# Optimization experiments

Measured on AMD Instinct MI355X. Metric: run time of the kernel, lower is better.

## Reference

```python
import jax, jax.numpy as jnp
import numpy as np

EPS = 1e-5

def _bn(x, p):
    # p: (4, C) rows = gamma, beta, running_mean, running_var ; x: (B, C, H, W)
    g, b, m, v = p[0], p[1], p[2], p[3]
    sh = (1, -1, 1, 1)
    return (x - m.reshape(sh)) * (g.reshape(sh) * jax.lax.rsqrt(v.reshape(sh) + EPS)) + b.reshape(sh)

def _cba1(x, w, p):
    # 1x1 conv (no bias) + BN + ReLU
    return jax.nn.relu(_bn(jnp.einsum('oc,bchw->bohw', w, x), p))

def setup_inputs() -> dict:
    B, C, H, W = 2, 512, 128, 256
    CK, K, CO = 256, 19, 512
    key = jax.random.key(0)
    ks = jax.random.split(key, 10)
    def w(k, shape, fan):
        return jax.random.normal(k, shape, jnp.float32) * (fan ** -0.5)
    def bn(c):
        return jnp.stack([jnp.ones((c,), jnp.float32), jnp.zeros((c,), jnp.float32),
                          jnp.zeros((c,), jnp.float32), jnp.ones((c,), jnp.float32)])
    return {
        'x': jax.random.normal(ks[0], (B, C, H, W), jnp.float32),
        'proxy_feats': jax.random.normal(ks[1], (B, C, K, 1), jnp.float32),
        'wq1': w(ks[2], (CK, C), C),  'bnq1': bn(CK),
        'wq2': w(ks[3], (CK, CK), CK), 'bnq2': bn(CK),
        'wk1': w(ks[4], (CK, C), C),  'bnk1': bn(CK),
        'wk2': w(ks[5], (CK, CK), CK), 'bnk2': bn(CK),
        'wv':  w(ks[6], (CK, C), C),  'bnv':  bn(CK),
        'wout': w(ks[7], (C, CK), CK), 'bnout': bn(C),
        'wbot': w(ks[8], (CO, 2 * C, 3, 3), 2 * C * 9), 'bnbot': bn(CO),
    }

def reference(x, proxy_feats, wq1, wq2, wk1, wk2, wv, wout, wbot,
              bnq1, bnq2, bnk1, bnk2, bnv, bnout, bnbot):
    B, C, H, W = x.shape
    CK = wq1.shape[0]
    # --- ObjectContextBlock: pixel-region cross attention ---
    q = _cba1(_cba1(x, wq1, bnq1), wq2, bnq2)            # (B, CK, H, W)
    k = _cba1(_cba1(proxy_feats, wk1, bnk1), wk2, bnk2)  # (B, CK, K, 1)
    v = _cba1(proxy_feats, wv, bnv)                      # (B, CK, K, 1)
    q = q.reshape(B, CK, H * W)                          # (B, CK, N)
    k = k.reshape(B, CK, -1)                             # (B, CK, K)
    v = v.reshape(B, CK, -1)                             # (B, CK, K)
    sim = jnp.einsum('bcn,bck->bnk', q, k) * (CK ** -0.5)
    sim = jax.nn.softmax(sim, axis=-1)                   # (B, N, K)
    ctx = jnp.einsum('bnk,bck->bcn', sim, v).reshape(B, CK, H, W)
    ctx = _cba1(ctx, wout, bnout)                        # (B, C, H, W)
    # --- bottleneck: concat + 3x3 conv + BN + ReLU ---
    cat = jnp.concatenate([ctx, x], axis=1)              # (B, 2C, H, W)
    out = jax.lax.conv_general_dilated(cat, wbot, (1, 1), 'SAME',
                                       dimension_numbers=('NCHW', 'OIHW', 'NCHW'))
    return jax.nn.relu(_bn(out, bnbot))
```

## Files before the change

### kernel.cpp

```cpp
#include <hip/hip_runtime.h>
#include <cstdint>

#define EPS 1e-5f
#define PADW 258
#define PADROWS 33540
#define NPIX 32768

typedef __attribute__((ext_vector_type(8))) short bf16x8;
typedef __attribute__((ext_vector_type(4))) float f32x4;

__device__ __forceinline__ ushort f2bf(float f) {
  union { float f; uint32_t u; } v; v.f = f;
  uint32_t r = v.u + 0x7fffu + ((v.u >> 16) & 1u);
  return (ushort)(r >> 16);
}
__device__ __forceinline__ float bf2f(ushort h) {
  union { uint32_t u; float f; } v; v.u = ((uint32_t)h) << 16;
  return v.f;
}
__device__ __forceinline__ void gload_lds16(const void* g, void* lds) {
  __builtin_amdgcn_global_load_lds((__attribute__((address_space(1))) void*)g,
                                   (__attribute__((address_space(3))) void*)lds,
                                   16, 0, 0);
}

template <int BMODE, int OMODE>
__global__ __launch_bounds__(256) void mfma_gemm(
    const ushort* __restrict__ A, const ushort* __restrict__ B,
    const float* __restrict__ bn, void* __restrict__ OutV,
    int M, int K, int pitchB, int ciB, long strideB, int pitchO, long strideO) {
  const int lane = threadIdx.x & 63;
  const int wave = threadIdx.x >> 6;
  const int wm = (wave & 1) * 64;
  const int wn = (wave >> 1) * 64;
  const int m0 = blockIdx.y * 128;
  const int n0 = blockIdx.x * 128;
  const int z  = blockIdx.z;
  B += (size_t)z * strideB;

  const int h = n0 >> 8, w0 = n0 & 255;
  long prowB;
  if (BMODE == 0) prowB = n0;
  else            prowB = (long)(h + 1) * PADW + (w0 + 1);

  __shared__ __align__(16) ushort Asl[4 * 128 * 8];
  __shared__ __align__(16) ushort Bsl[4 * 128 * 8];

  f32x4 acc[4][4];
#pragma unroll
  for (int mt = 0; mt < 4; ++mt)
#pragma unroll
    for (int nt = 0; nt < 4; ++nt) acc[mt][nt] = (f32x4){0.f, 0.f, 0.f, 0.f};

  for (int k0 = 0; k0 < K; k0 += 32) {
#pragma unroll
    for (int i = 0; i < 2; ++i) {
      int s = wave * 2 + i;
      int c = s * 64 + lane;
      int mm = c & 127, ks = c >> 7;
      gload_lds16(A + (size_t)(m0 + mm) * K + (k0 + ks * 8), Asl + s * 512);
    }
    long rowb; int cib;
    if (BMODE == 2) {
      int tap = k0 >> 10;
      int dy = tap / 3 - 1, dx = tap % 3 - 1;
      rowb = prowB + dy * PADW + dx;
      cib  = k0 & 1023;
    } else {
      rowb = prowB;
      cib  = ciB + k0;
    }
#pragma unroll
    for (int i = 0; i < 2; ++i) {
      int s = wave * 2 + i;
      int c = s * 64 + lane;
      int nn = c & 127, ks = c >> 7;
      gload_lds16(B + (size_t)(rowb + nn) * pitchB + cib + ks * 8, Bsl + s * 512);
    }
    __syncthreads();
    bf16x8 af[4], bfr[4];
#pragma unroll
    for (int t = 0; t < 4; ++t) {
      af[t]  = *(const bf16x8*)(Asl + (((lane >> 4) * 128) + wm + t * 16 + (lane & 15)) * 8);
      bfr[t] = *(const bf16x8*)(Bsl + (((lane >> 4) * 128) + wn + t * 16 + (lane & 15)) * 8);
    }
#pragma unroll
    for (int mt = 0; mt < 4; ++mt)
#pragma unroll
      for (int nt = 0; nt < 4; ++nt)
        acc[mt][nt] = __builtin_amdgcn_mfma_f32_16x16x32_bf16(af[mt], bfr[nt], acc[mt][nt], 0, 0, 0);
    __syncthreads();
  }

  const int q4 = lane >> 4, col = lane & 15;
  float scv[16], bov[16];
#pragma unroll
  for (int mt = 0; mt < 4; ++mt)
#pragma unroll
    for (int r = 0; r < 4; ++r) {
      int m = m0 + wm + mt * 16 + q4 * 4 + r;
      float s = bn[m] * rsqrtf(bn[3 * M + m] + EPS);
      scv[mt * 4 + r] = s;
      bov[mt * 4 + r] = bn[M + m] - bn[2 * M + m] * s;
    }
  if (OMODE == 2) {
    float* Outf = (float*)OutV + (size_t)z * strideO;
#pragma unroll
    for (int mt = 0; mt < 4; ++mt)
#pragma unroll
      for (int r = 0; r < 4; ++r) {
        int m = m0 + wm + mt * 16 + q4 * 4 + r;
        float* rowp = Outf + (size_t)m * NPIX + n0 + wn;
#pragma unroll
        for (int nt = 0; nt < 4; ++nt)
          rowp[nt * 16 + col] = fmaxf(acc[mt][nt][r] * scv[mt * 4 + r] + bov[mt * 4 + r], 0.f);
      }
  } else {
    ushort* Outh = (ushort*)OutV + (size_t)z * strideO;
    long prowO = (OMODE == 0) ? (long)n0 : ((long)(h + 1) * PADW + (w0 + 1));
#pragma unroll
    for (int nt = 0; nt < 4; ++nt) {
      long row = prowO + wn + nt * 16 + col;
      ushort* p = Outh + (size_t)row * pitchO + m0 + wm;
#pragma unroll
      for (int mt = 0; mt < 4; ++mt) {
        ushort4 pk;
        pk.x = f2bf(fmaxf(acc[mt][nt][0] * scv[mt * 4 + 0] + bov[mt * 4 + 0], 0.f));
        pk.y = f2bf(fmaxf(acc[mt][nt][1] * scv[mt * 4 + 1] + bov[mt * 4 + 1], 0.f));
        pk.z = f2bf(fmaxf(acc[mt][nt][2] * scv[mt * 4 + 2] + bov[mt * 4 + 2], 0.f));
        pk.w = f2bf(fmaxf(acc[mt][nt][3] * scv[mt * 4 + 3] + bov[mt * 4 + 3], 0.f));
        *(ushort4*)(p + mt * 16 + q4 * 4) = pk;
      }
    }
  }
}

#define PXS  130
#define ROWC (PXS * 4)
#define BUFC (3 * ROWC)
__global__ __launch_bounds__(256, 3) void conv3x3_mfma(
    const ushort* __restrict__ W2, const ushort* __restrict__ cat,
    const float* __restrict__ bn, float* __restrict__ out) {
  const int tid  = threadIdx.x;
  const int lane = tid & 63;
  const int wave = tid >> 6;
  const int wm = (wave & 1) * 64;
  const int wn = (wave >> 1) * 64;
  const int m0 = (blockIdx.x & 3) * 128;
  const int n0 = (blockIdx.x >> 2) * 128;
  const int z  = blockIdx.z;
  const int h = n0 >> 8, w0 = n0 & 255;
  const long prow0 = (long)(h + 1) * PADW + (w0 + 1);
  const ushort* Bz = cat + (size_t)z * PADROWS * 1024;

  __shared__ __align__(16) ushort halo[2 * BUFC * 8];

  f32x4 acc[4][4];
#pragma unroll
  for (int mt = 0; mt < 4; ++mt)
#pragma unroll
    for (int nt = 0; nt < 4; ++nt) acc[mt][nt] = (f32x4){0.f, 0.f, 0.f, 0.f};

  long offs[7];
#pragma unroll
  for (int s = 0; s < 7; ++s) {
    int c = s * 256 + tid;
    if (c < BUFC) {
      int o = c & 3;
      int q = c >> 2;
      int p = q % PXS;
      int r = q / PXS;
      offs[s] = ((prow0 + (long)(r - 1) * PADW + (p - 1)) << 10) + o * 8;
    } else {
      offs[s] = -1;
    }
  }

  auto stage = [&](int buf, int ci0n) {
#pragma unroll
    for (int s = 0; s < 7; ++s)
      if (offs[s] >= 0)
        gload_lds16(Bz + offs[s] + ci0n,
                    halo + ((size_t)buf * BUFC + s * 256 + wave * 64) * 8);
  };

  const ushort* Alane = W2 + (size_t)(m0 + wm + (lane & 15)) * 32 + (lane >> 4) * 8;
  const int hlane = 4 * (wn + (lane & 15)) + (lane >> 4);

  stage(0, 0);
  __syncthreads();

  for (int it = 0; it < 32; ++it) {
    if (it < 31) stage((it + 1) & 1, (it + 1) * 32);

    const ushort* Ait = Alane + (size_t)it * (9 * 16384);
    const ushort* hb0 = halo + (size_t)(it & 1) * BUFC * 8;
#pragma unroll
    for (int t = 0; t < 9; ++t) {
      bf16x8 af[4];
#pragma unroll
      for (int mt = 0; mt < 4; ++mt)
        af[mt] = *(const bf16x8*)(Ait + (size_t)t * 16384 + mt * 512);
      const int hb = hlane + (t / 3) * ROWC + (t % 3) * 4;
#pragma unroll
      for (int nt = 0; nt < 4; ++nt) {
        bf16x8 bfr = *(const bf16x8*)(hb0 + (size_t)(hb + nt * 64) * 8);
#pragma unroll
        for (int mt = 0; mt < 4; ++mt)
          acc[mt][nt] = __builtin_amdgcn_mfma_f32_16x16x32_bf16(af[mt], bfr, acc[mt][nt], 0, 0, 0);
      }
    }
    __syncthreads();
  }

  const int q4 = lane >> 4, col = lane & 15;
  float* Outf = out + (size_t)z * 512 * NPIX;
#pragma unroll
  for (int mt = 0; mt < 4; ++mt)
#pragma unroll
    for (int r = 0; r < 4; ++r) {
      int m = m0 + wm + mt * 16 + q4 * 4 + r;
      float s  = bn[m] * rsqrtf(bn[3 * 512 + m] + EPS);
      float bo = bn[512 + m] - bn[2 * 512 + m] * s;
      float* rowp = Outf + (size_t)m * NPIX + n0 + wn;
#pragma unroll
      for (int nt = 0; nt < 4; ++nt)
        rowp[nt * 16 + col] = fmaxf(acc[mt][nt][r] * s + bo, 0.f);
    }
}

__global__ __launch_bounds__(64) void small_gemm_kernel(
    const float* __restrict__ Wm, const float* __restrict__ X,
    const float* __restrict__ bn, float* __restrict__ Y,
    int CO, int CI, int KC) {
  int co = blockIdx.x, b = blockIdx.y, kc = threadIdx.x;
  if (kc >= KC) return;
  const float* Xb = X + (size_t)b * CI * KC;
  float acc = 0.f;
  for (int c = 0; c < CI; ++c) acc += Wm[(size_t)co * CI + c] * Xb[(size_t)c * KC + kc];
  float s  = bn[co] * rsqrtf(bn[3 * CO + co] + EPS);
  float bs = bn[CO + co] - bn[2 * CO + co] * s;
  Y[((size_t)b * CO + co) * KC + kc] = fmaxf(acc * s + bs, 0.f);
}

__global__ __launch_bounds__(256) void attention_kernel(
    const ushort* __restrict__ qT, const float* __restrict__ Kp,
    const float* __restrict__ Vp, ushort* __restrict__ ctxT) {
  int b = blockIdx.y;
  int pix = blockIdx.x * 256 + threadIdx.x;
  __shared__ float ks[256][19], vs[256][19];
  for (int idx = threadIdx.x; idx < 256 * 19; idx += 256) {
    int c = idx / 19, kk = idx % 19;
    ks[c][kk] = Kp[((size_t)b * 256 + c) * 19 + kk];
    vs[c][kk] = Vp[((size_t)b * 256 + c) * 19 + kk];
  }
  __syncthreads();

  const ushort* qrow = qT + ((size_t)b * NPIX + pix) * 256;
  float sim[19];
#pragma unroll
  for (int kk = 0; kk < 19; ++kk) sim[kk] = 0.f;
  for (int c0 = 0; c0 < 256; c0 += 8) {
    uint4 raw = *(const uint4*)(qrow + c0);
    float qf[8] = {bf2f((ushort)(raw.x & 0xffff)), bf2f((ushort)(raw.x >> 16)),
                   bf2f((ushort)(raw.y & 0xffff)), bf2f((ushort)(raw.y >> 16)),
                   bf2f((ushort)(raw.z & 0xffff)), bf2f((ushort)(raw.z >> 16)),
                   bf2f((ushort)(raw.w & 0xffff)), bf2f((ushort)(raw.w >> 16))};
#pragma unroll
    for (int j = 0; j < 8; ++j)
#pragma unroll
      for (int kk = 0; kk < 19; ++kk) sim[kk] += qf[j] * ks[c0 + j][kk];
  }
  const float scale = 0.0625f;
  float mx = -1e30f;
#pragma unroll
  for (int kk = 0; kk < 19; ++kk) { sim[kk] *= scale; mx = fmaxf(mx, sim[kk]); }
  float denom = 0.f;
#pragma unroll
  for (int kk = 0; kk < 19; ++kk) { sim[kk] = __expf(sim[kk] - mx); denom += sim[kk]; }
  float inv = 1.f / denom;
#pragma unroll
  for (int kk = 0; kk < 19; ++kk) sim[kk] *= inv;

  ushort* crow = ctxT + ((size_t)b * NPIX + pix) * 256;
  for (int c0 = 0; c0 < 256; c0 += 8) {
    uint32_t o[4];
#pragma unroll
    for (int j = 0; j < 4; ++j) {
      float v0 = 0.f, v1 = 0.f;
#pragma unroll
      for (int kk = 0; kk < 19; ++kk) {
        v0 += sim[kk] * vs[c0 + j * 2][kk];
        v1 += sim[kk] * vs[c0 + j * 2 + 1][kk];
      }
      o[j] = (uint32_t)f2bf(v0) | ((uint32_t)f2bf(v1) << 16);
    }
    *(uint4*)(crow + c0) = make_uint4(o[0], o[1], o[2], o[3]);
  }
}

__global__ __launch_bounds__(256) void transpose_x_kernel(
    const float* __restrict__ x, ushort* __restrict__ cat) {
  int b = blockIdx.z, ci0 = blockIdx.y * 64, n0 = blockIdx.x * 64;
  __shared__ float t[64][65];
  const float* xb = x + ((size_t)b * 512 + ci0) * NPIX + n0;
  for (int i = 0; i < 16; ++i) {
    int idx = i * 256 + threadIdx.x;
    int c = idx >> 6, w = idx & 63;
    t[c][w] = xb[(size_t)c * NPIX + w];
  }
  __syncthreads();
  int h = n0 >> 8, w0 = n0 & 255;
  size_t pbase = ((size_t)b * PADROWS + (size_t)(h + 1) * PADW + (w0 + 1)) * 1024 + 512 + ci0;
  for (int i = 0; i < 16; ++i) {
    int idx = i * 256 + threadIdx.x;
    int n = idx >> 6, c = idx & 63;
    cat[pbase + (size_t)n * 1024 + c] = f2bf(t[c][n]);
  }
}

__global__ void convert_w_kernel(const float* __restrict__ in, ushort* __restrict__ out, int n) {
  int i = blockIdx.x * 256 + threadIdx.x;
  if (i < n) out[i] = f2bf(in[i]);
}
__global__ void repack_conv_w_kernel(const float* __restrict__ wbot, ushort* __restrict__ Wrb) {
  int idx = blockIdx.x * 256 + threadIdx.x;
  if (idx >= 512 * 9216) return;
  int ci_in = idx & 31;
  int r  = idx >> 5;
  int co = r & 511;
  int tt = r >> 9;
  int t = tt % 9, chunk = tt / 9;
  Wrb[idx] = f2bf(wbot[((size_t)co * 1024 + chunk * 32 + ci_in) * 9 + t]);
}

extern "C" void kernel_launch(void* const* d_in, const int* in_sizes, int n_in,
                              void* d_out, int out_size, void* d_ws, size_t ws_size,
                              hipStream_t stream) {
  const float* x     = (const float*)d_in[0];
  const float* proxy = (const float*)d_in[1];
  const float* wq1   = (const float*)d_in[2];
  const float* bnq1  = (const float*)d_in[3];
  const float* wq2   = (const float*)d_in[4];
  const float* bnq2  = (const float*)d_in[5];
  const float* wk1   = (const float*)d_in[6];
  const float* bnk1  = (const float*)d_in[7];
  const float* wk2   = (const float*)d_in[8];
  const float* bnk2  = (const float*)d_in[9];
  const float* wv    = (const float*)d_in[10];
  const float* bnv   = (const float*)d_in[11];
  const float* wout  = (const float*)d_in[12];
  const float* bnout = (const float*)d_in[13];
  const float* wbot  = (const float*)d_in[14];
  const float* bnbot = (const float*)d_in[15];
  float* out = (float*)d_out;

  const int B = 2, C = 512, CK = 256, KC = 19;
  char* ws = (char*)d_ws;
  const size_t catBytes = (size_t)B * PADROWS * 1024 * 2;
  ushort* cat  = (ushort*)ws;
  ushort* bufA = (ushort*)(ws + 137379840);
  ushort* bufB = (ushort*)(ws + 137379840 + 33554432);
  ushort* Wrb  = (ushort*)(ws + 204488704);
  ushort* wq1b = (ushort*)(ws + 213925888);
  ushort* wq2b = (ushort*)(ws + 214188032);
  ushort* woutb= (ushort*)(ws + 214319104);
  float*  k1   = (float*)(ws + 214581248);
  float*  k2   = k1 + (size_t)B * CK * KC;
  float*  vv   = k2 + (size_t)B * CK * KC;

  hipMemsetAsync(cat, 0, catBytes, stream);

  convert_w_kernel<<<(CK * C + 255) / 256, 256, 0, stream>>>(wq1, wq1b, CK * C);
  convert_w_kernel<<<(CK * CK + 255) / 256, 256, 0, stream>>>(wq2, wq2b, CK * CK);
  convert_w_kernel<<<(C * CK + 255) / 256, 256, 0, stream>>>(wout, woutb, C * CK);
  repack_conv_w_kernel<<<(512 * 9216 + 255) / 256, 256, 0, stream>>>(wbot, Wrb);

  small_gemm_kernel<<<dim3(CK, B), 64, 0, stream>>>(wk1, proxy, bnk1, k1, CK, C, KC);
  small_gemm_kernel<<<dim3(CK, B), 64, 0, stream>>>(wk2, k1, bnk2, k2, CK, CK, KC);
  small_gemm_kernel<<<dim3(CK, B), 64, 0, stream>>>(wv, proxy, bnv, vv, CK, C, KC);

  transpose_x_kernel<<<dim3(NPIX / 64, 8, B), 256, 0, stream>>>(x, cat);

  const long padStride = (long)PADROWS * 1024;
  const long nckStride = (long)NPIX * 256;

  mfma_gemm<1, 0><<<dim3(NPIX / 128, 2, B), 256, 0, stream>>>(
      wq1b, cat, bnq1, bufA, 256, 512, 1024, 512, padStride, 256, nckStride);
  mfma_gemm<0, 0><<<dim3(NPIX / 128, 2, B), 256, 0, stream>>>(
      wq2b, bufA, bnq2, bufB, 256, 256, 256, 0, nckStride, 256, nckStride);

  attention_kernel<<<dim3(NPIX / 256, B), 256, 0, stream>>>(bufB, k2, vv, bufA);

  mfma_gemm<0, 1><<<dim3(NPIX / 128, 4, B), 256, 0, stream>>>(
      woutb, bufA, bnout, cat, 512, 256, 256, 0, nckStride, 1024, padStride);

  conv3x3_mfma<<<dim3((NPIX / 128) * 4, 1, B), 256, 0, stream>>>(Wrb, cat, bnbot, out);
}
```

Baseline: 1.302 ms.

## Swizzle halo LDS layout and prefetch weight fragments in 3x3 conv loop

Adds an XOR swizzle on the 16-byte octet slot inside each halo pixel row, applied both when global data is staged into LDS and when B fragments are read back. This is meant to cut LDS bank conflicts. Weight A fragments are now loaded from global three taps ahead in a rotating buffer, and the async staging is wrapped in sched barriers so the loads overlap with MFMA work. MFMA bursts also run at raised wave priority. The cost is more registers, which may lower occupancy.

```diff
diff --git a/kernel.cpp b/kernel.cpp
--- a/kernel.cpp
+++ b/kernel.cpp
@@ -166,11 +166,12 @@
   for (int s = 0; s < 7; ++s) {
     int c = s * 256 + tid;
     if (c < BUFC) {
-      int o = c & 3;
+      int o_slot = c & 3;
       int q = c >> 2;
       int p = q % PXS;
       int r = q / PXS;
-      offs[s] = ((prow0 + (long)(r - 1) * PADW + (p - 1)) << 10) + o * 8;
+      int o_g = o_slot ^ ((p >> 1) & 3);
+      offs[s] = ((prow0 + (long)(r - 1) * PADW + (p - 1)) << 10) + o_g * 8;
     } else {
       offs[s] = -1;
     }
@@ -185,29 +186,55 @@
   };
 
   const ushort* Alane = W2 + (size_t)(m0 + wm + (lane & 15)) * 32 + (lane >> 4) * 8;
-  const int hlane = 4 * (wn + (lane & 15)) + (lane >> 4);
+
+  const int p0  = wn + (lane & 15);
+  const int oct = lane >> 4;
+  int hoff[12];
+#pragma unroll
+  for (int nt = 0; nt < 4; ++nt)
+#pragma unroll
+    for (int dx = 0; dx < 3; ++dx) {
+      int p = p0 + nt * 16 + dx;
+      hoff[nt * 3 + dx] = (p * 4 + (oct ^ ((p >> 1) & 3))) * 16;
+    }
 
   stage(0, 0);
   __syncthreads();
 
   for (int it = 0; it < 32; ++it) {
+    const ushort* Ait = Alane + (size_t)it * (9 * 16384);
+
+    bf16x8 af[3][4];
+#pragma unroll
+    for (int t = 0; t < 3; ++t)
+#pragma unroll
+      for (int mt = 0; mt < 4; ++mt)
+        af[t][mt] = *(const bf16x8*)(Ait + (size_t)t * 16384 + mt * 512);
+
+    __builtin_amdgcn_sched_barrier(0);
     if (it < 31) stage((it + 1) & 1, (it + 1) * 32);
-
-    const ushort* Ait = Alane + (size_t)it * (9 * 16384);
-    const ushort* hb0 = halo + (size_t)(it & 1) * BUFC * 8;
+    __builtin_amdgcn_sched_barrier(0);
+
+    const char* hb0 = (const char*)(halo + (size_t)(it & 1) * BUFC * 8);
 #pragma unroll
     for (int t = 0; t < 9; ++t) {
-      bf16x8 af[4];
-#pragma unroll
-      for (int mt = 0; mt < 4; ++mt)
-        af[mt] = *(const bf16x8*)(Ait + (size_t)t * 16384 + mt * 512);
-      const int hb = hlane + (t / 3) * ROWC + (t % 3) * 4;
-#pragma unroll
-      for (int nt = 0; nt < 4; ++nt) {
-        bf16x8 bfr = *(const bf16x8*)(hb0 + (size_t)(hb + nt * 64) * 8);
+      const int slot = t % 3;
+      const int r = t / 3, dx = t % 3;
+      bf16x8 bfr[4];
+#pragma unroll
+      for (int nt = 0; nt < 4; ++nt)
+        bfr[nt] = *(const bf16x8*)(hb0 + r * (ROWC * 16) + hoff[nt * 3 + dx]);
+      __builtin_amdgcn_s_setprio(1);
+#pragma unroll
+      for (int nt = 0; nt < 4; ++nt)
 #pragma unroll
         for (int mt = 0; mt < 4; ++mt)
-          acc[mt][nt] = __builtin_amdgcn_mfma_f32_16x16x32_bf16(af[mt], bfr, acc[mt][nt], 0, 0, 0);
+          acc[mt][nt] = __builtin_amdgcn_mfma_f32_16x16x32_bf16(af[slot][mt], bfr[nt], acc[mt][nt], 0, 0, 0);
+      __builtin_amdgcn_s_setprio(0);
+      if (t < 6) {
+#pragma unroll
+        for (int mt = 0; mt < 4; ++mt)
+          af[slot][mt] = *(const bf16x8*)(Ait + (size_t)(t + 3) * 16384 + mt * 512);
       }
     }
     __syncthreads();
```

Result: no change. 1.300 ms (-0.2%).
